# Optimization experiments

Hardware: AMD Instinct MI355X
Metric: run time of the kernel (lower is better)

Reference implementation:

```python
import jax, jax.numpy as jnp
import numpy as np
from jax import lax

PROP_TIME = 18
K_F = 3
NUM = K_F * K_F - 1   # 8 non-center taps
IDX_REF = NUM // 2    # 4


def _bilinear(img, ys, xs):
    """img: (H,W). ys/xs: (T,H,W) absolute coords. Zero padding outside."""
    H, W = img.shape
    y0 = jnp.floor(ys)
    x0 = jnp.floor(xs)
    wy = ys - y0
    wx = xs - x0
    y0i = y0.astype(jnp.int32)
    x0i = x0.astype(jnp.int32)

    def g(yi, xi):
        valid = (yi >= 0) & (yi < H) & (xi >= 0) & (xi < W)
        v = img[jnp.clip(yi, 0, H - 1), jnp.clip(xi, 0, W - 1)]
        return jnp.where(valid, v, 0.0)

    v00 = g(y0i, x0i)
    v01 = g(y0i, x0i + 1)
    v10 = g(y0i + 1, x0i)
    v11 = g(y0i + 1, x0i + 1)
    return (v00 * (1 - wy) * (1 - wx) + v01 * (1 - wy) * wx
            + v10 * wy * (1 - wx) + v11 * wy * wx)


_sample_b = jax.vmap(_bilinear, in_axes=(0, 0, 0))  # batched over B


def setup_inputs() -> dict:
    key = jax.random.key(0)
    k1, k2, k3, k4, k5 = jax.random.split(key, 5)
    B, H, W = 4, 480, 640
    CH_G = 8
    return {
        "feat_init": jax.random.uniform(k1, (B, 1, H, W), dtype=jnp.float32),
        "guidance": jax.random.normal(k2, (B, CH_G, H, W), dtype=jnp.float32),
        "confidence": jax.random.uniform(k3, (B, 1, H, W), dtype=jnp.float32),
        "w_oa": jax.random.normal(k4, (3 * NUM, CH_G, 3, 3), dtype=jnp.float32) * 0.1,
        "b_oa": jax.random.normal(k5, (3 * NUM,), dtype=jnp.float32) * 0.01,
        "aff_scale_const": jnp.ones((1,), jnp.float32) * (0.5 * NUM),  # gamma*num (TGASS)
    }


def reference(feat_init, guidance, confidence, w_oa, b_oa, aff_scale_const):
    B, _, H, W = guidance.shape

    # offset / affinity head: Conv2d(ch_g, 3*num, k=3, pad=1)
    oa = lax.conv_general_dilated(
        guidance, w_oa, window_strides=(1, 1), padding=((1, 1), (1, 1)),
        dimension_numbers=("NCHW", "OIHW", "NCHW")) + b_oa[None, :, None, None]
    o1, o2, aff = jnp.split(oa, 3, axis=1)  # each (B, 8, H, W): dy, dx, raw aff

    # insert zero offset for the center (reference) tap -> 9 taps
    z = jnp.zeros((B, 1, H, W), o1.dtype)
    off_y = jnp.concatenate([o1[:, :IDX_REF], z, o1[:, IDX_REF:]], axis=1)  # (B,9,H,W)
    off_x = jnp.concatenate([o2[:, :IDX_REF], z, o2[:, IDX_REF:]], axis=1)

    # TGASS affinity
    aff = jnp.tanh(aff) / (aff_scale_const + 1e-8)

    # confidence propagation: 1x1 deform conv per non-center tap with w_conf=1,
    # modulation=1 -> bilinear sample of confidence at p + offset (offset detached)
    nc = jnp.array([0, 1, 2, 3, 5, 6, 7, 8])
    base_y = jnp.arange(H, dtype=jnp.float32)[:, None]
    base_x = jnp.arange(W, dtype=jnp.float32)[None, :]
    yc = base_y[None, None] + lax.stop_gradient(off_y[:, nc])  # (B,8,H,W)
    xc = base_x[None, None] + lax.stop_gradient(off_x[:, nc])
    conf_aff = _sample_b(confidence[:, 0], yc, xc)             # (B,8,H,W)
    aff = aff * conf_aff

    # absolute-sum normalization (TGASS: clamp denom at 1)
    s = jnp.sum(jnp.abs(aff), axis=1, keepdims=True) + 1e-4
    s = jnp.maximum(s, 1.0)
    aff = aff / s
    aff_ref = 1.0 - jnp.sum(aff, axis=1, keepdims=True)
    aff9 = jnp.concatenate([aff[:, :IDX_REF], aff_ref, aff[:, IDX_REF:]], axis=1)
    aff9 = jax.nn.softmax(aff9, axis=1)  # (B,9,H,W)

    # propagation sampling coords: p + kernel_tap + learned offset (fixed per iter)
    kh = jnp.repeat(jnp.arange(-1, 2, dtype=jnp.float32), 3)  # (9,)
    kw = jnp.tile(jnp.arange(-1, 2, dtype=jnp.float32), 3)
    ys = base_y[None, None] + kh[None, :, None, None] + off_y  # (B,9,H,W)
    xs = base_x[None, None] + kw[None, :, None, None] + off_x

    def step(feat, _):
        samp = _sample_b(feat[:, 0], ys, xs)                  # (B,9,H,W)
        new = jnp.sum(aff9 * samp, axis=1, keepdims=True)     # (B,1,H,W)
        return new, None

    feat_result, _ = lax.scan(step, feat_init, None, length=PROP_TIME)
    return feat_result
```

## Files before the change

### kernel.cpp

```cpp
#include <hip/hip_runtime.h>
#include <hip/hip_fp16.h>
#include <math.h>

#define BB 4
#define HH 480
#define WW 640
#define HW (HH * WW)
#define PP (BB * HW)

#define PXT 5
#define NBLK (PP / (256 * PXT))

__device__ __forceinline__ float ldz(const float* __restrict__ img, int y, int x) {
    bool v = ((unsigned)y < (unsigned)HH) & ((unsigned)x < (unsigned)WW);
    int off = v ? (y * WW + x) : 0;
    float val = img[off];
    return v ? val : 0.0f;
}

__device__ __forceinline__ void axis_map(int y0, float wy, int H,
                                         int& c0, float& t, float& s) {
    if (y0 >= 0 && y0 <= H - 2)      { c0 = y0;    t = wy;   s = 1.0f; }
    else if (y0 == -1)               { c0 = 0;     t = 0.0f; s = wy; }
    else if (y0 == H - 1)            { c0 = H - 2; t = 1.0f; s = 1.0f - wy; }
    else                             { c0 = 0;     t = 0.0f; s = 0.0f; }
}

__device__ __forceinline__ float tanh_fast(float x) {
    return 1.0f - 2.0f / (__expf(2.0f * x) + 1.0f);
}

__global__ void transpose_w_kernel(const float* __restrict__ w_oa, float* __restrict__ wT) {
    for (int i = threadIdx.x; i < 1728; i += 256) {
        const int k = i / 192;
        const int r = i - k * 192;
        const int ci = r / 24;
        const int c = r - ci * 24;
        wT[i] = w_oa[c * 72 + ci * 9 + k];
    }
}

__global__ __launch_bounds__(256) void precompute_kernel(
    const float* __restrict__ guidance,
    const float* __restrict__ confidence,
    const float* __restrict__ wT,
    const float* __restrict__ b_oa,
    const float* __restrict__ aff_scale,
    uint4* __restrict__ PK4,
    float* __restrict__ affC)
{
    const int p = blockIdx.x * 256 + threadIdx.x;
    const int b = p / HW;
    const int rem = p - b * HW;
    const int y = rem / WW;
    const int x = rem - y * WW;

    float acc[24];
    #pragma unroll
    for (int c = 0; c < 24; ++c) acc[c] = b_oa[c];

    const float* gb = guidance + (size_t)b * 8 * HW;

    #pragma unroll 1
    for (int kidx = 0; kidx < 9; ++kidx) {
        const int yy = y + kidx / 3 - 1;
        const int xx = x + kidx % 3 - 1;
        const bool valid = ((unsigned)yy < (unsigned)HH) & ((unsigned)xx < (unsigned)WW);
        const int base = valid ? (yy * WW + xx) : 0;
        float g[8];
        #pragma unroll
        for (int ci = 0; ci < 8; ++ci) {
            float v = gb[ci * HW + base];
            g[ci] = valid ? v : 0.0f;
        }
        const float* wk = wT + kidx * 192;
        #pragma unroll
        for (int ci = 0; ci < 8; ++ci) {
            const float gv = g[ci];
            #pragma unroll
            for (int c = 0; c < 24; ++c)
                acc[c] = fmaf(gv, wk[ci * 24 + c], acc[c]);
        }
    }

    const float inv_scale = 1.0f / (aff_scale[0] + 1e-8f);
    const float* cb = confidence + (size_t)b * HW;
    const float fy = (float)y, fx = (float)x;

    float affv[8];
    #pragma unroll
    for (int j = 0; j < 8; ++j) {
        const float oy = acc[j], ox = acc[8 + j];
        const float a = tanh_fast(acc[16 + j]) * inv_scale;
        const float ysj = fy + oy, xsj = fx + ox;
        const float y0f = floorf(ysj), x0f = floorf(xsj);
        const float wy = ysj - y0f, wx = xsj - x0f;
        const int y0 = (int)y0f, x0 = (int)x0f;
        const float v00 = ldz(cb, y0, x0),     v01 = ldz(cb, y0, x0 + 1);
        const float v10 = ldz(cb, y0 + 1, x0), v11 = ldz(cb, y0 + 1, x0 + 1);
        const float conf = v00 * (1.0f - wy) * (1.0f - wx) + v01 * (1.0f - wy) * wx
                         + v10 * wy * (1.0f - wx)          + v11 * wy * wx;
        affv[j] = a * conf;
    }

    float s = 1e-4f;
    #pragma unroll
    for (int j = 0; j < 8; ++j) s += fabsf(affv[j]);
    s = fmaxf(s, 1.0f);
    const float inv_s = 1.0f / s;
    float sum = 0.0f;
    #pragma unroll
    for (int j = 0; j < 8; ++j) { affv[j] *= inv_s; sum += affv[j]; }
    const float aref = 1.0f - sum;

    float m = aref;
    #pragma unroll
    for (int j = 0; j < 8; ++j) m = fmaxf(m, affv[j]);
    float e[8];
    float denom = 0.0f;
    #pragma unroll
    for (int j = 0; j < 8; ++j) { e[j] = __expf(affv[j] - m); denom += e[j]; }
    const float ec = __expf(aref - m);
    denom += ec;
    const float invden = 1.0f / denom;

    affC[p] = ec * invden * 8192.0f;

    unsigned ba[8], tt[8];
    #pragma unroll
    for (int j = 0; j < 8; ++j) {
        const int t9 = (j < 4) ? j : j + 1;
        const float khv = (float)(t9 / 3 - 1);
        const float kwv = (float)(t9 % 3 - 1);
        const float ys = (fy + khv) + acc[j];
        const float xs = (fx + kwv) + acc[8 + j];
        const float y0f = floorf(ys), x0f = floorf(xs);
        const float wy = ys - y0f, wx = xs - x0f;
        int y0c, x0c; float ty, tx, sy, sx;
        axis_map((int)y0f, wy, HH, y0c, ty, sy);
        axis_map((int)x0f, wx, WW, x0c, tx, sx);

        const float aeff = (e[j] * invden) * sy * sx;
        unsigned aq = __float2uint_rn(aeff * 8192.0f);
        aq = aq > 8191u ? 8191u : aq;
        ba[j] = ((unsigned)(y0c * WW + x0c) << 13) | aq;
        __half2 h2 = __floats2half2_rn(ty, tx);
        tt[j] = __builtin_bit_cast(unsigned, h2);
    }
    PK4[4 * p + 0] = make_uint4(ba[0], tt[0], ba[1], tt[1]);
    PK4[4 * p + 1] = make_uint4(ba[2], tt[2], ba[3], tt[3]);
    PK4[4 * p + 2] = make_uint4(ba[4], tt[4], ba[5], tt[5]);
    PK4[4 * p + 3] = make_uint4(ba[6], tt[6], ba[7], tt[7]);
}

__global__ __launch_bounds__(256) void prop_kernel(
    const float* __restrict__ src,
    float* __restrict__ dst,
    const uint4* __restrict__ PK4,
    const float* __restrict__ affC)
{
    const int tid = threadIdx.x;
    const int p0 = blockIdx.x * (256 * PXT) + tid;
    const float* fb = src + (p0 / HW) * HW;

    #pragma unroll
    for (int k = 0; k < PXT; ++k) {
        const int p = p0 + k * 256;
        const uint4 q0 = PK4[4 * p + 0];
        const uint4 q1 = PK4[4 * p + 1];
        const uint4 q2 = PK4[4 * p + 2];
        const uint4 q3 = PK4[4 * p + 3];

        float acc = affC[p] * src[p];

        auto tap = [&](unsigned bav, unsigned tw) {
            const float af = (float)(bav & 8191u);
            const float* g = fb + (bav >> 13);
            const float2 t2 = *reinterpret_cast<const float2*>(g);
            const float2 b2 = *reinterpret_cast<const float2*>(g + WW);
            const float2 t = __half22float2(__builtin_bit_cast(__half2, tw));
            const float top = fmaf(t.y, t2.y - t2.x, t2.x);
            const float bot = fmaf(t.y, b2.y - b2.x, b2.x);
            acc = fmaf(af, fmaf(t.x, bot - top, top), acc);
        };
        tap(q0.x, q0.y); tap(q0.z, q0.w);
        tap(q1.x, q1.y); tap(q1.z, q1.w);
        tap(q2.x, q2.y); tap(q2.z, q2.w);
        tap(q3.x, q3.y); tap(q3.z, q3.w);

        dst[p] = acc * (1.0f / 8192.0f);
    }
}

extern "C" void kernel_launch(void* const* d_in, const int* in_sizes, int n_in,
                              void* d_out, int out_size, void* d_ws, size_t ws_size,
                              hipStream_t stream) {
    const float* feat_init  = (const float*)d_in[0];
    const float* guidance   = (const float*)d_in[1];
    const float* confidence = (const float*)d_in[2];
    const float* w_oa       = (const float*)d_in[3];
    const float* b_oa       = (const float*)d_in[4];
    const float* aff_scale  = (const float*)d_in[5];
    float* out = (float*)d_out;
    float* ws  = (float*)d_ws;

    const size_t need = (size_t)18 * PP * sizeof(float);
    if (ws_size < need) return;

    uint4* PK4  = reinterpret_cast<uint4*>(ws);
    float* affC = ws + (size_t)16 * PP;
    float* bufA = ws + (size_t)17 * PP;
    float* wT   = bufA;

    transpose_w_kernel<<<1, 256, 0, stream>>>(w_oa, wT);
    precompute_kernel<<<PP / 256, 256, 0, stream>>>(guidance, confidence, wT, b_oa,
                                                    aff_scale, PK4, affC);

    const float* srcp = feat_init;
    for (int i = 0; i < 18; ++i) {
        float* dstp = (i & 1) ? out : bufA;
        prop_kernel<<<NBLK, 256, 0, stream>>>(srcp, dstp, PK4, affC);
        srcp = dstp;
    }
}
```

Measured before the change: 615.8 us.

## Split packed tap data into planar arrays, use nontemporal loads and block swizzle

```diff
diff --git a/kernel.cpp b/kernel.cpp
--- a/kernel.cpp
+++ b/kernel.cpp
@@ -8,8 +8,9 @@
 #define HW (HH * WW)
 #define PP (BB * HW)
 
-#define PXT 5
-#define NBLK (PP / (256 * PXT))
+#define PROP_NBLK (PP / 256)
+
+typedef unsigned u32x4 __attribute__((ext_vector_type(4)));
 
 __device__ __forceinline__ float ldz(const float* __restrict__ img, int y, int x) {
     bool v = ((unsigned)y < (unsigned)HH) & ((unsigned)x < (unsigned)WW);
@@ -46,7 +47,8 @@
     const float* __restrict__ wT,
     const float* __restrict__ b_oa,
     const float* __restrict__ aff_scale,
-    uint4* __restrict__ PK4,
+    u32x4* __restrict__ PKa, u32x4* __restrict__ PKb,
+    u32x4* __restrict__ PKc, u32x4* __restrict__ PKd,
     float* __restrict__ affC)
 {
     const int p = blockIdx.x * 256 + threadIdx.x;
@@ -147,49 +149,47 @@
         __half2 h2 = __floats2half2_rn(ty, tx);
         tt[j] = __builtin_bit_cast(unsigned, h2);
     }
-    PK4[4 * p + 0] = make_uint4(ba[0], tt[0], ba[1], tt[1]);
-    PK4[4 * p + 1] = make_uint4(ba[2], tt[2], ba[3], tt[3]);
-    PK4[4 * p + 2] = make_uint4(ba[4], tt[4], ba[5], tt[5]);
-    PK4[4 * p + 3] = make_uint4(ba[6], tt[6], ba[7], tt[7]);
+    PKa[p] = (u32x4){ba[0], tt[0], ba[1], tt[1]};
+    PKb[p] = (u32x4){ba[2], tt[2], ba[3], tt[3]};
+    PKc[p] = (u32x4){ba[4], tt[4], ba[5], tt[5]};
+    PKd[p] = (u32x4){ba[6], tt[6], ba[7], tt[7]};
 }
 
 __global__ __launch_bounds__(256) void prop_kernel(
     const float* __restrict__ src,
     float* __restrict__ dst,
-    const uint4* __restrict__ PK4,
+    const u32x4* __restrict__ PKa, const u32x4* __restrict__ PKb,
+    const u32x4* __restrict__ PKc, const u32x4* __restrict__ PKd,
     const float* __restrict__ affC)
 {
-    const int tid = threadIdx.x;
-    const int p0 = blockIdx.x * (256 * PXT) + tid;
-    const float* fb = src + (p0 / HW) * HW;
-
-    #pragma unroll
-    for (int k = 0; k < PXT; ++k) {
-        const int p = p0 + k * 256;
-        const uint4 q0 = PK4[4 * p + 0];
-        const uint4 q1 = PK4[4 * p + 1];
-        const uint4 q2 = PK4[4 * p + 2];
-        const uint4 q3 = PK4[4 * p + 3];
-
-        float acc = affC[p] * src[p];
-
-        auto tap = [&](unsigned bav, unsigned tw) {
-            const float af = (float)(bav & 8191u);
-            const float* g = fb + (bav >> 13);
-            const float2 t2 = *reinterpret_cast<const float2*>(g);
-            const float2 b2 = *reinterpret_cast<const float2*>(g + WW);
-            const float2 t = __half22float2(__builtin_bit_cast(__half2, tw));
-            const float top = fmaf(t.y, t2.y - t2.x, t2.x);
-            const float bot = fmaf(t.y, b2.y - b2.x, b2.x);
-            acc = fmaf(af, fmaf(t.x, bot - top, top), acc);
-        };
-        tap(q0.x, q0.y); tap(q0.z, q0.w);
-        tap(q1.x, q1.y); tap(q1.z, q1.w);
-        tap(q2.x, q2.y); tap(q2.z, q2.w);
-        tap(q3.x, q3.y); tap(q3.z, q3.w);
-
-        dst[p] = acc * (1.0f / 8192.0f);
-    }
+    const int bid = (blockIdx.x & 7) * (PROP_NBLK / 8) + (blockIdx.x >> 3);
+    const int p = bid * 256 + threadIdx.x;
+    const float* fb = src + (p / HW) * HW;
+
+    const u32x4 qa = __builtin_nontemporal_load(&PKa[p]);
+    const u32x4 qb = __builtin_nontemporal_load(&PKb[p]);
+    const u32x4 qc = __builtin_nontemporal_load(&PKc[p]);
+    const u32x4 qd = __builtin_nontemporal_load(&PKd[p]);
+    const float ac = __builtin_nontemporal_load(&affC[p]);
+
+    float acc = ac * src[p];
+
+    auto tap = [&](unsigned bav, unsigned tw) {
+        const float af = (float)(bav & 8191u);
+        const float* g = fb + (bav >> 13);
+        const float2 t2 = *reinterpret_cast<const float2*>(g);
+        const float2 b2 = *reinterpret_cast<const float2*>(g + WW);
+        const float2 t = __half22float2(__builtin_bit_cast(__half2, tw));
+        const float top = fmaf(t.y, t2.y - t2.x, t2.x);
+        const float bot = fmaf(t.y, b2.y - b2.x, b2.x);
+        acc = fmaf(af, fmaf(t.x, bot - top, top), acc);
+    };
+    tap(qa.x, qa.y); tap(qa.z, qa.w);
+    tap(qb.x, qb.y); tap(qb.z, qb.w);
+    tap(qc.x, qc.y); tap(qc.z, qc.w);
+    tap(qd.x, qd.y); tap(qd.z, qd.w);
+
+    dst[p] = acc * (1.0f / 8192.0f);
 }
 
 extern "C" void kernel_launch(void* const* d_in, const int* in_sizes, int n_in,
@@ -207,19 +207,22 @@
     const size_t need = (size_t)18 * PP * sizeof(float);
     if (ws_size < need) return;
 
-    uint4* PK4  = reinterpret_cast<uint4*>(ws);
+    u32x4* PKa  = reinterpret_cast<u32x4*>(ws);
+    u32x4* PKb  = reinterpret_cast<u32x4*>(ws + (size_t)4 * PP);
+    u32x4* PKc  = reinterpret_cast<u32x4*>(ws + (size_t)8 * PP);
+    u32x4* PKd  = reinterpret_cast<u32x4*>(ws + (size_t)12 * PP);
     float* affC = ws + (size_t)16 * PP;
     float* bufA = ws + (size_t)17 * PP;
     float* wT   = bufA;
 
     transpose_w_kernel<<<1, 256, 0, stream>>>(w_oa, wT);
     precompute_kernel<<<PP / 256, 256, 0, stream>>>(guidance, confidence, wT, b_oa,
-                                                    aff_scale, PK4, affC);
+                                                    aff_scale, PKa, PKb, PKc, PKd, affC);
 
     const float* srcp = feat_init;
     for (int i = 0; i < 18; ++i) {
         float* dstp = (i & 1) ? out : bufA;
-        prop_kernel<<<NBLK, 256, 0, stream>>>(srcp, dstp, PK4, affC);
+        prop_kernel<<<PROP_NBLK, 256, 0, stream>>>(srcp, dstp, PKa, PKb, PKc, PKd, affC);
         srcp = dstp;
     }
 }
```

Measured after the change: 542.4 us. 11.9% less time.
